# Optimization experiments

Measured on AMD Instinct MI355X. Metric: run time of the kernel, lower is better.

## Reference

```python
import jax, jax.numpy as jnp
import numpy as np

RBF_START = 0.0
RBF_END = 10.0
RBF_STEPS = 32
OUT_SIZE = 64
ENERGY_SCALE = 1.0

L, R, T = 128, 1024, 16  # lig atoms, rec atoms, transform hypotheses


def setup_inputs() -> dict:
    key = jax.random.key(0)
    k1, k2, k3, k4 = jax.random.split(key, 4)
    return {
        "lig_feat": jax.random.normal(k1, (L, RBF_STEPS, OUT_SIZE), dtype=jnp.float32),
        "rec_feat": jax.random.normal(k2, (R, RBF_STEPS, OUT_SIZE), dtype=jnp.float32),
        "lig_coords": jax.random.normal(k3, (T, L, 3), dtype=jnp.float32),  # transformed lig coords per hypothesis
        "rec_coords": jax.random.normal(k4, (R, 3), dtype=jnp.float32),
    }


def reference(lig_feat, rec_feat, lig_coords, rec_coords):
    # attention coefficients: [L, R, E] where E = rbf_steps
    atn = jnp.einsum('lef,ref->lre', lig_feat, rec_feat)

    mu = jnp.linspace(RBF_START, RBF_END, RBF_STEPS, dtype=jnp.float32)  # [E]
    sigma = (RBF_START - RBF_END) / RBF_STEPS  # matches original (sign irrelevant, squared)

    # pairwise distances per transform: [T, L, R]
    diff = lig_coords[:, :, None, :] - rec_coords[None, None, :, :]  # [T, L, R, 3]
    dists = jnp.sqrt(jnp.sum(diff * diff, axis=-1))  # [T, L, R]

    # RBF encode: [T, L, R, E]
    rbf = jnp.exp(-(((dists[..., None] - mu) / sigma) ** 2))

    # attention-weighted energy reduction per transform: [T]
    Us = jnp.einsum('lre,tlre->t', atn, rbf) * ENERGY_SCALE
    return Us
```

## Files before the change

### kernel.cpp

```cpp
#include <hip/hip_runtime.h>
#include <hip/hip_bf16.h>

#define L_CNT 128
#define R_CNT 1024
#define T_CNT 16
#define E_CNT 32
#define F_CNT 64

constexpr float SFAC    = 3.8435917f;
constexpr float MUS     = SFAC * (10.0f / 31.0f);
constexpr float INV_MUS = 1.0f / MUS;

#if defined(__has_builtin)
#  if __has_builtin(__builtin_amdgcn_exp2f)
#    define EXP2(x) __builtin_amdgcn_exp2f(x)
#  endif
#endif
#ifndef EXP2
#  define EXP2(x) exp2f(x)
#endif

typedef __attribute__((ext_vector_type(8))) short short8_t;
typedef __attribute__((ext_vector_type(4))) float f32x4;

__device__ __forceinline__ short f2bf(float f) {
    __bf16 h = (__bf16)f;
    return __builtin_bit_cast(short, h);
}

#define PADK 72
__global__ __launch_bounds__(256) void atn_mfma(const float* __restrict__ lig,
                                                const float* __restrict__ rec,
                                                unsigned short* __restrict__ atn) {
    const int e   = blockIdx.x;
    const int l0  = blockIdx.y * 64;
    const int r0  = blockIdx.z * 128;
    const int tid = threadIdx.x;

    __shared__ __align__(16) short As[64 * PADK];
    __shared__ __align__(16) short Bs[128 * PADK];

#pragma unroll
    for (int i = 0; i < 4; ++i) {
        int idx = i * 256 + tid;
        int row = idx >> 4;
        int f4  = idx & 15;
        float4 v = *(const float4*)(lig + ((size_t)(l0 + row) * 32 + e) * 64 + f4 * 4);
        short4 p;
        p.x = f2bf(v.x); p.y = f2bf(v.y); p.z = f2bf(v.z); p.w = f2bf(v.w);
        *(short4*)(&As[row * PADK + f4 * 4]) = p;
    }
#pragma unroll
    for (int i = 0; i < 8; ++i) {
        int idx = i * 256 + tid;
        int row = idx >> 4;
        int f4  = idx & 15;
        float4 v = *(const float4*)(rec + ((size_t)(r0 + row) * 32 + e) * 64 + f4 * 4);
        short4 p;
        p.x = f2bf(v.x); p.y = f2bf(v.y); p.z = f2bf(v.z); p.w = f2bf(v.w);
        *(short4*)(&Bs[row * PADK + f4 * 4]) = p;
    }
    __syncthreads();

    const int wave = tid >> 6;
    const int lane = tid & 63;
    const int fr   = lane & 15;
    const int kg   = lane >> 4;

    f32x4 acc[8];
#pragma unroll
    for (int n = 0; n < 8; ++n) acc[n] = (f32x4){0.f, 0.f, 0.f, 0.f};

    short8_t a0 = *(short8_t*)(&As[(16 * wave + fr) * PADK + kg * 8]);
    short8_t a1 = *(short8_t*)(&As[(16 * wave + fr) * PADK + 32 + kg * 8]);

#pragma unroll
    for (int n = 0; n < 8; ++n) {
        short8_t b0 = *(short8_t*)(&Bs[(16 * n + fr) * PADK + kg * 8]);
        short8_t b1 = *(short8_t*)(&Bs[(16 * n + fr) * PADK + 32 + kg * 8]);
        acc[n] = __builtin_amdgcn_mfma_f32_16x16x32_bf16(a0, b0, acc[n], 0, 0, 0);
        acc[n] = __builtin_amdgcn_mfma_f32_16x16x32_bf16(a1, b1, acc[n], 0, 0, 0);
    }

    const int orow = l0 + 16 * wave + (lane >> 4) * 4;
    const int ocol = r0 + fr;
#pragma unroll
    for (int n = 0; n < 8; ++n) {
#pragma unroll
        for (int j = 0; j < 4; ++j) {
            size_t off = ((size_t)e * 128 + orow + j) * 1024 + ocol + 16 * n;
            atn[off] = (unsigned short)f2bf(acc[n][j]);
        }
    }
}

__global__ __launch_bounds__(256) void energy_kernel(const unsigned short* __restrict__ atn,
                                                     const float* __restrict__ ligc,
                                                     const float* __restrict__ recc,
                                                     float* __restrict__ partials) {
    __shared__ unsigned int atn_sd[E_CNT * 128];
    const unsigned short* atn_su = (const unsigned short*)atn_sd;

    const int tid   = threadIdx.x;
    const int l     = blockIdx.x >> 2;
    const int rbase = (blockIdx.x & 3) * 256;
    const int r     = rbase + tid;

    const unsigned int* atn_d = (const unsigned int*)atn;
    unsigned int stage[16];
#pragma unroll
    for (int it = 0; it < 16; ++it) {
        int idx = it * 256 + tid;
        int e   = idx >> 7;
        int rh  = idx & 127;
        stage[it] = atn_d[(size_t)e * 65536 + (size_t)l * 512 + (rbase >> 1) + rh];
    }

    const float rx = recc[r * 3 + 0];
    const float ry = recc[r * 3 + 1];
    const float rz = recc[r * 3 + 2];

    float d[T_CNT];
#pragma unroll
    for (int t = 0; t < T_CNT; ++t) {
        float dx = ligc[((size_t)t * 128 + l) * 3 + 0] - rx;
        float dy = ligc[((size_t)t * 128 + l) * 3 + 1] - ry;
        float dz = ligc[((size_t)t * 128 + l) * 3 + 2] - rz;
        d[t] = sqrtf(dx * dx + dy * dy + dz * dz);
    }

#pragma unroll
    for (int it = 0; it < 16; ++it) atn_sd[it * 256 + tid] = stage[it];
    __syncthreads();

    float acc[T_CNT];
#pragma unroll
    for (int t = 0; t < T_CNT; ++t) acc[t] = 0.0f;

#pragma unroll
    for (int t = 0; t < T_CNT; ++t) {
        const float u   = d[t] * SFAC;
        float e0f = rintf(u * INV_MUS);
        e0f = fminf(fmaxf(e0f, 3.0f), 28.0f);
        const int   em3 = (int)e0f - 3;
        const float um  = fmaf(e0f, -MUS, u);
#pragma unroll
        for (int k = 0; k < 7; ++k) {
            const float w  = um - (float)(k - 3) * MUS;
            const float ae = __uint_as_float((unsigned)atn_su[(em3 + k) * 256 + tid] << 16);
            acc[t] = fmaf(ae, EXP2(-(w * w)), acc[t]);
        }
    }

    __shared__ float red[4][T_CNT];
    const int lane = tid & 63;
    const int wid  = tid >> 6;
#pragma unroll
    for (int t = 0; t < T_CNT; ++t) {
#pragma unroll
        for (int m = 32; m >= 1; m >>= 1) acc[t] += __shfl_xor(acc[t], m, 64);
    }
    if (lane == 0) {
#pragma unroll
        for (int t = 0; t < T_CNT; ++t) red[wid][t] = acc[t];
    }
    __syncthreads();
    if (tid < T_CNT) {
        float s = red[0][tid] + red[1][tid] + red[2][tid] + red[3][tid];
        partials[(size_t)blockIdx.x * T_CNT + tid] = s;
    }
}

__global__ __launch_bounds__(256) void final_reduce(const float* __restrict__ partials,
                                                    float* __restrict__ out) {
    __shared__ float red[16][17];
    const int t = threadIdx.x & 15;
    const int g = threadIdx.x >> 4;
    float s = 0.0f;
    for (int b = g; b < 512; b += 16) s += partials[(size_t)b * 16 + t];
    red[g][t] = s;
    __syncthreads();
    if (threadIdx.x < 16) {
        float v = 0.0f;
#pragma unroll
        for (int g2 = 0; g2 < 16; ++g2) v += red[g2][threadIdx.x];
        out[threadIdx.x] = v;
    }
}

extern "C" void kernel_launch(void* const* d_in, const int* in_sizes, int n_in,
                              void* d_out, int out_size, void* d_ws, size_t ws_size,
                              hipStream_t stream) {
    const float* lig  = (const float*)d_in[0];
    const float* rec  = (const float*)d_in[1];
    const float* ligc = (const float*)d_in[2];
    const float* recc = (const float*)d_in[3];
    float* out = (float*)d_out;

    unsigned short* atn = (unsigned short*)d_ws;
    float* partials = (float*)((char*)d_ws + (size_t)E_CNT * L_CNT * R_CNT * 2);

    atn_mfma<<<dim3(E_CNT, 2, 8), 256, 0, stream>>>(lig, rec, atn);
    energy_kernel<<<512, 256, 0, stream>>>(atn, ligc, recc, partials);
    final_reduce<<<1, 256, 0, stream>>>(partials, out);
}
```

Before: 28.08 us.

## Stage MFMA output through swizzled LDS and shrink RBF window to five bins

The attention GEMM kernel now writes its bf16 results into a swizzled shared-memory tile that reuses the input buffers, then stores 16-byte vectors to global memory instead of scattered 2-byte stores. The energy kernel narrows the truncated RBF window from 7 to 5 neighbouring bins around the nearest centre, cutting exp2 and LDS reads per transform. The narrower window drops Gaussian terms with larger offsets, which adds approximation error to the energy sum.

```diff
diff --git a/kernel.cpp b/kernel.cpp
--- a/kernel.cpp
+++ b/kernel.cpp
@@ -5,7 +5,6 @@
 #define R_CNT 1024
 #define T_CNT 16
 #define E_CNT 32
-#define F_CNT 64
 
 constexpr float SFAC    = 3.8435917f;
 constexpr float MUS     = SFAC * (10.0f / 31.0f);
@@ -29,6 +28,8 @@
 }
 
 #define PADK 72
+#define CPAD 136
+
 __global__ __launch_bounds__(256) void atn_mfma(const float* __restrict__ lig,
                                                 const float* __restrict__ rec,
                                                 unsigned short* __restrict__ atn) {
@@ -37,8 +38,10 @@
     const int r0  = blockIdx.z * 128;
     const int tid = threadIdx.x;
 
-    __shared__ __align__(16) short As[64 * PADK];
-    __shared__ __align__(16) short Bs[128 * PADK];
+    __shared__ __align__(16) short smem[64 * PADK + 128 * PADK];
+    short* As = smem;
+    short* Bs = smem + 64 * PADK;
+    short* Cs = smem;
 
 #pragma unroll
     for (int i = 0; i < 4; ++i) {
@@ -81,16 +84,27 @@
         acc[n] = __builtin_amdgcn_mfma_f32_16x16x32_bf16(a0, b0, acc[n], 0, 0, 0);
         acc[n] = __builtin_amdgcn_mfma_f32_16x16x32_bf16(a1, b1, acc[n], 0, 0, 0);
     }
-
-    const int orow = l0 + 16 * wave + (lane >> 4) * 4;
-    const int ocol = r0 + fr;
+    __syncthreads();
+
+    const int orow_l = 16 * wave + (lane >> 4) * 4;
+    const int sw_w   = ((orow_l >> 2) & 3) << 4;
 #pragma unroll
     for (int n = 0; n < 8; ++n) {
 #pragma unroll
         for (int j = 0; j < 4; ++j) {
-            size_t off = ((size_t)e * 128 + orow + j) * 1024 + ocol + 16 * n;
-            atn[off] = (unsigned short)f2bf(acc[n][j]);
+            Cs[(orow_l + j) * CPAD + ((16 * n + fr) ^ sw_w)] = f2bf(acc[n][j]);
         }
+    }
+    __syncthreads();
+
+#pragma unroll
+    for (int it2 = 0; it2 < 4; ++it2) {
+        int idx = it2 * 256 + tid;
+        int row = idx >> 4;
+        int c8  = idx & 15;
+        int sw  = ((row >> 2) & 3) << 4;
+        short8_t v = *(short8_t*)(&Cs[row * CPAD + ((c8 * 8) ^ sw)]);
+        *(short8_t*)(&atn[((size_t)e * 128 + l0 + row) * 1024 + r0 + c8 * 8]) = v;
     }
 }
 
@@ -100,6 +114,7 @@
                                                      float* __restrict__ partials) {
     __shared__ unsigned int atn_sd[E_CNT * 128];
     const unsigned short* atn_su = (const unsigned short*)atn_sd;
+    __shared__ float red[4][T_CNT];
 
     const int tid   = threadIdx.x;
     const int l     = blockIdx.x >> 2;
@@ -111,9 +126,9 @@
 #pragma unroll
     for (int it = 0; it < 16; ++it) {
         int idx = it * 256 + tid;
-        int e   = idx >> 7;
+        int ee  = idx >> 7;
         int rh  = idx & 127;
-        stage[it] = atn_d[(size_t)e * 65536 + (size_t)l * 512 + (rbase >> 1) + rh];
+        stage[it] = atn_d[(size_t)ee * 65536 + (size_t)l * 512 + (rbase >> 1) + rh];
     }
 
     const float rx = recc[r * 3 + 0];
@@ -139,20 +154,19 @@
 
 #pragma unroll
     for (int t = 0; t < T_CNT; ++t) {
-        const float u   = d[t] * SFAC;
+        const float u = d[t] * SFAC;
         float e0f = rintf(u * INV_MUS);
-        e0f = fminf(fmaxf(e0f, 3.0f), 28.0f);
-        const int   em3 = (int)e0f - 3;
+        e0f = fminf(fmaxf(e0f, 2.0f), 29.0f);
+        const int   em2 = (int)e0f - 2;
         const float um  = fmaf(e0f, -MUS, u);
 #pragma unroll
-        for (int k = 0; k < 7; ++k) {
-            const float w  = um - (float)(k - 3) * MUS;
-            const float ae = __uint_as_float((unsigned)atn_su[(em3 + k) * 256 + tid] << 16);
+        for (int k = 0; k < 5; ++k) {
+            const float w  = um - (float)(k - 2) * MUS;
+            const float ae = __uint_as_float((unsigned)atn_su[(em2 + k) * 256 + tid] << 16);
             acc[t] = fmaf(ae, EXP2(-(w * w)), acc[t]);
         }
     }
 
-    __shared__ float red[4][T_CNT];
     const int lane = tid & 63;
     const int wid  = tid >> 6;
 #pragma unroll
```

New measurement: 27.38 us. 1.03x faster.
